# Kernel tuning notes

Hardware: AMD Instinct MI355X
Metric: run time of the kernel (lower is better)

Reference implementation:

```python
import jax, jax.numpy as jnp
import numpy as np

K_V = 0.5
G_OFF = 0.001
G_ON = 0.005
N_IN = 4096
N_OUT = 4096
BATCH = 8192


def setup_inputs() -> dict:
    key = jax.random.key(0)
    k1, k2, k3 = jax.random.split(key, 3)
    x = jax.random.normal(k1, (BATCH, N_IN), dtype=jnp.float32)
    # RandomNormal(stddev=1/sqrt(neurons_in)) initializer
    w = jax.random.normal(k2, (N_IN, N_OUT), dtype=jnp.float32) / np.sqrt(N_IN)
    # bias initialized to 0 in the module; use small noise so it is non-degenerate
    b = jax.random.normal(k3, (N_OUT,), dtype=jnp.float32) * 0.01
    return {"x": x, "w": w, "b": b}


def reference(x, w, b):
    # combine_weights: fold bias as an extra input row, x gets a ones column
    weights = jnp.concatenate([w, b[None, :]], axis=0)            # (n_in+1, n_out)
    ones = jnp.ones((x.shape[0], 1), dtype=x.dtype)
    voltages = K_V * jnp.concatenate([x, ones], axis=1)           # (B, n_in+1)

    # weights_to_conductances, 'lowest' mapping rule (differential pair)
    max_weight = jnp.max(jnp.abs(weights))
    k_cond = (G_ON - G_OFF) / max_weight
    g_eff = k_cond * weights
    g_pos = G_OFF + jnp.maximum(g_eff, 0.0)                       # even columns
    g_neg = G_OFF - jnp.minimum(g_eff, 0.0)                       # odd columns
    # interleave pos/neg -> (n_in+1, 2*n_out)
    conductances = jnp.stack([g_pos, g_neg], axis=-1).reshape(weights.shape[0], -1)

    # crossbar currents: scaled GEMM
    currents = voltages @ conductances                            # (B, 2*n_out)

    # differential current subtraction + rescale back to weight domain
    total_currents = currents[:, 0::2] - currents[:, 1::2]        # (B, n_out)
    y_disturbed = total_currents / (K_V * k_cond)
    return y_disturbed
```

## Files before the change

### kernel.cpp

```cpp
#include <hip/hip_runtime.h>
#include <cstdint>

typedef unsigned short u16;
typedef __attribute__((ext_vector_type(8))) __bf16 bf16x8;
typedef __attribute__((ext_vector_type(4))) float f32x4;

#define M_DIM 8192
#define N_DIM 4096
#define K_DIM 4096

#define CVT_X_BLOCKS 16384
#define CVT_W_BLOCKS 4096

__device__ __forceinline__ u16 f2bf(float f) {
    union { float f; uint32_t u; } v; v.f = f;
    uint32_t u = v.u;
    u += 0x7FFFu + ((u >> 16) & 1u);
    return (u16)(u >> 16);
}

__global__ __launch_bounds__(256) void cvt_kernel(const float* __restrict__ x,
                                                  const float* __restrict__ w,
                                                  u16* __restrict__ xb,
                                                  u16* __restrict__ wt) {
    const int t = threadIdx.x;
    if (blockIdx.x < CVT_X_BLOCKS) {
        size_t i = ((size_t)blockIdx.x * 256 + t) * 8;
        const float4* p = (const float4*)(x + i);
        float4 v0 = p[0], v1 = p[1];
        uint32_t o0 = (uint32_t)f2bf(v0.x) | ((uint32_t)f2bf(v0.y) << 16);
        uint32_t o1 = (uint32_t)f2bf(v0.z) | ((uint32_t)f2bf(v0.w) << 16);
        uint32_t o2 = (uint32_t)f2bf(v1.x) | ((uint32_t)f2bf(v1.y) << 16);
        uint32_t o3 = (uint32_t)f2bf(v1.z) | ((uint32_t)f2bf(v1.w) << 16);
        uint4 o; o.x = o0; o.y = o1; o.z = o2; o.w = o3;
        *(uint4*)(xb + i) = o;
    } else {
        __shared__ u16 lds[64 * 68];
        const int bid = blockIdx.x - CVT_X_BLOCKS;
        const int k0 = (bid & 63) * 64;
        const int n0 = (bid >> 6) * 64;
#pragma unroll
        for (int i = 0; i < 4; ++i) {
            int idx = i * 256 + t;
            int r = idx >> 4;
            int c4 = (idx & 15) * 4;
            float4 v = *(const float4*)&w[(size_t)(k0 + r) * N_DIM + n0 + c4];
            uint2 o;
            o.x = (uint32_t)f2bf(v.x) | ((uint32_t)f2bf(v.y) << 16);
            o.y = (uint32_t)f2bf(v.z) | ((uint32_t)f2bf(v.w) << 16);
            *(uint2*)&lds[r * 68 + c4] = o;
        }
        __syncthreads();
#pragma unroll
        for (int i = 0; i < 4; ++i) {
            int idx = i * 256 + t;
            int rn  = idx >> 4;
            int ck  = (idx & 15) * 4;
            uint2 o;
            o.x = (uint32_t)lds[(ck + 0) * 68 + rn] | ((uint32_t)lds[(ck + 1) * 68 + rn] << 16);
            o.y = (uint32_t)lds[(ck + 2) * 68 + rn] | ((uint32_t)lds[(ck + 3) * 68 + rn] << 16);
            *(uint2*)&wt[(size_t)(n0 + rn) * K_DIM + k0 + ck] = o;
        }
    }
}

typedef const uint32_t __attribute__((address_space(1)))* gp_t;
typedef uint32_t __attribute__((address_space(3)))* lp_t;

__global__ __launch_bounds__(256) void gemm_kernel(const u16* __restrict__ A,
                                                   const u16* __restrict__ Bt,
                                                   const float* __restrict__ bias,
                                                   float* __restrict__ C) {
    __shared__ u16 As[128 * 32];
    __shared__ u16 Bs[128 * 32];

    const int t    = threadIdx.x;
    const int lane = t & 63;
    const int l16  = lane & 15;
    const int quad = lane >> 4;
    const int wave = t >> 6;
    const int wm   = (wave >> 1) * 64;
    const int wn   = (wave & 1) * 64;
    const int bm   = blockIdx.y * 128;
    const int bn   = blockIdx.x * 128;

    f32x4 acc[4][4] = {};

    const int c0 = t, c1 = 256 + t;
    const int rA0 = c0 >> 2, rA1 = c1 >> 2;
    const int sw  = ((rA0 >> 1) & 3);
    const int kc  = ((c0 & 3) ^ sw) * 8;
    const u16* a0 = A  + (size_t)(bm + rA0) * K_DIM + kc;
    const u16* a1 = A  + (size_t)(bm + rA1) * K_DIM + kc;
    const u16* b0 = Bt + (size_t)(bn + rA0) * K_DIM + kc;
    const u16* b1 = Bt + (size_t)(bn + rA1) * K_DIM + kc;

    const int sw8 = (quad ^ ((l16 >> 1) & 3)) * 8;

    for (int k0 = 0; k0 < K_DIM; k0 += 32) {
        __syncthreads();
        __builtin_amdgcn_global_load_lds((gp_t)(a0 + k0), (lp_t)&As[c0 * 8], 16, 0, 0);
        __builtin_amdgcn_global_load_lds((gp_t)(a1 + k0), (lp_t)&As[c1 * 8], 16, 0, 0);
        __builtin_amdgcn_global_load_lds((gp_t)(b0 + k0), (lp_t)&Bs[c0 * 8], 16, 0, 0);
        __builtin_amdgcn_global_load_lds((gp_t)(b1 + k0), (lp_t)&Bs[c1 * 8], 16, 0, 0);
        __syncthreads();

        bf16x8 af[4], bf[4];
#pragma unroll
        for (int i = 0; i < 4; ++i) {
            af[i] = *(const bf16x8*)&As[(wm + i * 16 + l16) * 32 + sw8];
            bf[i] = *(const bf16x8*)&Bs[(wn + i * 16 + l16) * 32 + sw8];
        }
#pragma unroll
        for (int i = 0; i < 4; ++i)
#pragma unroll
            for (int j = 0; j < 4; ++j)
                acc[i][j] = __builtin_amdgcn_mfma_f32_16x16x32_bf16(af[i], bf[j], acc[i][j], 0, 0, 0);
    }

#pragma unroll
    for (int j = 0; j < 4; ++j) {
        const int col = bn + wn + j * 16 + l16;
        const float bv = bias[col];
#pragma unroll
        for (int i = 0; i < 4; ++i) {
            const int row = bm + wm + i * 16 + quad * 4;
#pragma unroll
            for (int r = 0; r < 4; ++r)
                C[(size_t)(row + r) * N_DIM + col] = acc[i][j][r] + bv;
        }
    }
}

extern "C" void kernel_launch(void* const* d_in, const int* in_sizes, int n_in,
                              void* d_out, int out_size, void* d_ws, size_t ws_size,
                              hipStream_t stream) {
    const float* x = (const float*)d_in[0];
    const float* w = (const float*)d_in[1];
    const float* b = (const float*)d_in[2];
    float* out = (float*)d_out;

    u16* xb = (u16*)d_ws;
    u16* wt = xb + (size_t)M_DIM * K_DIM;

    cvt_kernel<<<CVT_X_BLOCKS + CVT_W_BLOCKS, 256, 0, stream>>>(x, w, xb, wt);
    gemm_kernel<<<dim3(N_DIM / 128, M_DIM / 128), 256, 0, stream>>>(xb, wt, b, out);
}
```

Before: 567.5 us.

## Enlarge GEMM tile to 256x256 with double-buffered LDS pipeline

Replaces the 128x128 tile, single-buffer GEMM with a 256x256 tile computed by 8 waves. Each wave accumulates a 128x64 sub-tile, and BK=64 is split into two 32-wide halves. Global-to-LDS loads for the next tile are issued while MFMAs run on the current buffer, synchronised with partial vmcnt waits. The change also adds a block-id swizzle for L2 locality and raises wave priority around MFMA bursts. The aim is to hide load latency and cut the per-iteration barrier cost, at the price of 128 KB LDS and heavy register use, which may limit occupancy.

```diff
diff --git a/kernel.cpp b/kernel.cpp
--- a/kernel.cpp
+++ b/kernel.cpp
@@ -67,69 +67,126 @@
 typedef const uint32_t __attribute__((address_space(1)))* gp_t;
 typedef uint32_t __attribute__((address_space(3)))* lp_t;
 
-__global__ __launch_bounds__(256) void gemm_kernel(const u16* __restrict__ A,
-                                                   const u16* __restrict__ Bt,
-                                                   const float* __restrict__ bias,
-                                                   float* __restrict__ C) {
-    __shared__ u16 As[128 * 32];
-    __shared__ u16 Bs[128 * 32];
+#define BK 64
+#define NTILES (K_DIM / BK)
+#define TN_TILES (N_DIM / 256)
+#define NWG ((M_DIM / 256) * TN_TILES)
+
+__global__ __launch_bounds__(512, 2) void gemm_kernel(const u16* __restrict__ A,
+                                                      const u16* __restrict__ Bt,
+                                                      const float* __restrict__ bias,
+                                                      float* __restrict__ C) {
+    __shared__ u16 As[2][2][256][32];
+    __shared__ u16 Bs[2][2][256][32];
 
     const int t    = threadIdx.x;
     const int lane = t & 63;
     const int l16  = lane & 15;
     const int quad = lane >> 4;
     const int wave = t >> 6;
-    const int wm   = (wave >> 1) * 64;
-    const int wn   = (wave & 1) * 64;
-    const int bm   = blockIdx.y * 128;
-    const int bn   = blockIdx.x * 128;
-
-    f32x4 acc[4][4] = {};
-
-    const int c0 = t, c1 = 256 + t;
-    const int rA0 = c0 >> 2, rA1 = c1 >> 2;
-    const int sw  = ((rA0 >> 1) & 3);
-    const int kc  = ((c0 & 3) ^ sw) * 8;
-    const u16* a0 = A  + (size_t)(bm + rA0) * K_DIM + kc;
-    const u16* a1 = A  + (size_t)(bm + rA1) * K_DIM + kc;
-    const u16* b0 = Bt + (size_t)(bn + rA0) * K_DIM + kc;
-    const u16* b1 = Bt + (size_t)(bn + rA1) * K_DIM + kc;
+    const int wr   = wave >> 2;
+    const int wc   = wave & 3;
+
+    const int bid = blockIdx.x;
+    const int wg  = (bid & 7) * (NWG >> 3) + (bid >> 3);
+    const int bm  = (wg / TN_TILES) * 256;
+    const int bn  = (wg % TN_TILES) * 256;
+
+    const int rC0 = t >> 2;
+    const int rC1 = rC0 + 128;
+    const int kcS = ((t & 3) ^ ((rC0 >> 1) & 3)) * 8;
+    const u16* a0 = A  + (size_t)(bm + rC0) * K_DIM + kcS;
+    const u16* a1 = A  + (size_t)(bm + rC1) * K_DIM + kcS;
+    const u16* b0 = Bt + (size_t)(bn + rC0) * K_DIM + kcS;
+    const u16* b1 = Bt + (size_t)(bn + rC1) * K_DIM + kcS;
 
     const int sw8 = (quad ^ ((l16 >> 1) & 3)) * 8;
 
-    for (int k0 = 0; k0 < K_DIM; k0 += 32) {
-        __syncthreads();
-        __builtin_amdgcn_global_load_lds((gp_t)(a0 + k0), (lp_t)&As[c0 * 8], 16, 0, 0);
-        __builtin_amdgcn_global_load_lds((gp_t)(a1 + k0), (lp_t)&As[c1 * 8], 16, 0, 0);
-        __builtin_amdgcn_global_load_lds((gp_t)(b0 + k0), (lp_t)&Bs[c0 * 8], 16, 0, 0);
-        __builtin_amdgcn_global_load_lds((gp_t)(b1 + k0), (lp_t)&Bs[c1 * 8], 16, 0, 0);
-        __syncthreads();
-
-        bf16x8 af[4], bf[4];
-#pragma unroll
-        for (int i = 0; i < 4; ++i) {
-            af[i] = *(const bf16x8*)&As[(wm + i * 16 + l16) * 32 + sw8];
-            bf[i] = *(const bf16x8*)&Bs[(wn + i * 16 + l16) * 32 + sw8];
-        }
-#pragma unroll
-        for (int i = 0; i < 4; ++i)
-#pragma unroll
-            for (int j = 0; j < 4; ++j)
-                acc[i][j] = __builtin_amdgcn_mfma_f32_16x16x32_bf16(af[i], bf[j], acc[i][j], 0, 0, 0);
+    f32x4 acc[8][4] = {};
+    bf16x8 af[4], bf[4];
+
+#define STAGE_A(buf, kh, kk) do {                                                                   \
+        __builtin_amdgcn_global_load_lds((gp_t)(a0 + (kk) + (kh) * 32), (lp_t)&As[buf][kh][rC0][(t & 3) * 8], 16, 0, 0); \
+        __builtin_amdgcn_global_load_lds((gp_t)(a1 + (kk) + (kh) * 32), (lp_t)&As[buf][kh][rC1][(t & 3) * 8], 16, 0, 0); \
+    } while (0)
+#define STAGE_B(buf, kh, kk) do {                                                                   \
+        __builtin_amdgcn_global_load_lds((gp_t)(b0 + (kk) + (kh) * 32), (lp_t)&Bs[buf][kh][rC0][(t & 3) * 8], 16, 0, 0); \
+        __builtin_amdgcn_global_load_lds((gp_t)(b1 + (kk) + (kh) * 32), (lp_t)&Bs[buf][kh][rC1][(t & 3) * 8], 16, 0, 0); \
+    } while (0)
+#define LDA(buf, kh, mbase)                                                                \
+    _Pragma("unroll")                                                                      \
+    for (int i = 0; i < 4; ++i)                                                            \
+        af[i] = *(const bf16x8*)&As[buf][kh][wr * 128 + ((mbase) + i) * 16 + l16][sw8]
+#define LDB(buf, kh)                                                                       \
+    _Pragma("unroll")                                                                      \
+    for (int j = 0; j < 4; ++j)                                                            \
+        bf[j] = *(const bf16x8*)&Bs[buf][kh][wc * 64 + j * 16 + l16][sw8]
+#define MFMA16(mbase)                                                                      \
+    __builtin_amdgcn_s_setprio(1);                                                         \
+    _Pragma("unroll")                                                                      \
+    for (int i = 0; i < 4; ++i)                                                            \
+        _Pragma("unroll")                                                                  \
+        for (int j = 0; j < 4; ++j)                                                        \
+            acc[(mbase) + i][j] =                                                          \
+                __builtin_amdgcn_mfma_f32_16x16x32_bf16(af[i], bf[j], acc[(mbase) + i][j], 0, 0, 0); \
+    __builtin_amdgcn_s_setprio(0)
+#define FENCE() asm volatile("" ::: "memory")
+
+    STAGE_A(0, 0, 0); STAGE_B(0, 0, 0);
+    STAGE_A(0, 1, 0); STAGE_B(0, 1, 0);
+    asm volatile("s_waitcnt vmcnt(4)" ::: "memory");
+    __builtin_amdgcn_s_barrier();
+    FENCE();
+
+#pragma unroll 2
+    for (int tt = 0; tt < NTILES; ++tt) {
+        const int nb = tt & 1;
+        const int pb = nb ^ 1;
+        const int kn = (tt + 1 < NTILES) ? (tt + 1) * BK : 0;
+
+        STAGE_A(pb, 0, kn);
+        LDB(nb, 0);
+        LDA(nb, 0, 0);
+        MFMA16(0);
+        STAGE_B(pb, 0, kn);
+        LDA(nb, 0, 4);
+        MFMA16(4);
+
+        asm volatile("s_waitcnt vmcnt(4)" ::: "memory");
+        __builtin_amdgcn_s_barrier();
+        FENCE();
+
+        STAGE_A(pb, 1, kn);
+        LDB(nb, 1);
+        LDA(nb, 1, 0);
+        MFMA16(0);
+        STAGE_B(pb, 1, kn);
+        LDA(nb, 1, 4);
+        MFMA16(4);
+
+        asm volatile("s_waitcnt vmcnt(4)" ::: "memory");
+        __builtin_amdgcn_s_barrier();
+        FENCE();
     }
 
 #pragma unroll
     for (int j = 0; j < 4; ++j) {
-        const int col = bn + wn + j * 16 + l16;
+        const int col = bn + wc * 64 + j * 16 + l16;
         const float bv = bias[col];
 #pragma unroll
-        for (int i = 0; i < 4; ++i) {
-            const int row = bm + wm + i * 16 + quad * 4;
+        for (int i = 0; i < 8; ++i) {
+            const int row = bm + wr * 128 + i * 16 + quad * 4;
 #pragma unroll
             for (int r = 0; r < 4; ++r)
                 C[(size_t)(row + r) * N_DIM + col] = acc[i][j][r] + bv;
         }
     }
+#undef STAGE_A
+#undef STAGE_B
+#undef LDA
+#undef LDB
+#undef MFMA16
+#undef FENCE
 }
 
 extern "C" void kernel_launch(void* const* d_in, const int* in_sizes, int n_in,
@@ -144,5 +201,5 @@
     u16* wt = xb + (size_t)M_DIM * K_DIM;
 
     cvt_kernel<<<CVT_X_BLOCKS + CVT_W_BLOCKS, 256, 0, stream>>>(x, w, xb, wt);
-    gemm_kernel<<<dim3(N_DIM / 128, M_DIM / 128), 256, 0, stream>>>(xb, wt, b, out);
-}
+    gemm_kernel<<<dim3(NWG), 512, 0, stream>>>(xb, wt, b, out);
+}
```

Result: faster. 538.4 us (-5.1%).
